# Performance work log

Hardware: AMD Instinct MI355X
Metric: run time of the kernel (lower is better)

The kernel has to match this reference:

```python
import jax, jax.numpy as jnp
import numpy as np

B, S, D = 256, 512, 128
NQ, NC, NQD, NCD = 20000, 2000, 101, 101


def setup_inputs() -> dict:
    key = jax.random.key(0)
    ks = jax.random.split(key, 32)
    s = 0.05
    inp = {
        "question_seq": jax.random.randint(ks[0], (B, S), 0, NQ),
        "concept_seq": jax.random.randint(ks[1], (B, S), 0, NC),
        "question_diff_seq": jax.random.randint(ks[2], (B, S), 0, NQD),
        "concept_diff_seq": jax.random.randint(ks[3], (B, S), 0, NCD),
        "correct_seq": jax.random.randint(ks[4], (B, S), 0, 2),
        "E_q": jax.random.normal(ks[5], (NQ, D)) * s,
        "E_c": jax.random.normal(ks[6], (NC, D)) * s,
        "E_qd": jax.random.normal(ks[7], (NQD, D)) * s,
        "E_cd": jax.random.normal(ks[8], (NCD, D)) * s,
        "E_corr": jax.random.normal(ks[9], (2, D)) * s,
        "Wx": jax.random.normal(ks[10], (4 * D, D)) * s,
        "bx": jnp.zeros((D,)),
        "W_s1": jax.random.normal(ks[11], (D, D)) * s,
        "b_s1": jnp.zeros((D,)),
        "W_s2": jax.random.normal(ks[12], (D, D)) * s,
        "b_s2": jnp.zeros((D,)),
        "W_p1": jax.random.normal(ks[13], (2 * D, D)) * s,
        "b_p1": jnp.zeros((D,)),
        "W_p2": jax.random.normal(ks[14], (2 * D, D)) * s,
        "b_p2": jnp.zeros((D,)),
        "W_ki": jax.random.normal(ks[15], (4 * D, D)) * s,
        "b_ki": jnp.zeros((D,)),
        # xavier_uniform init of h_pre: bound = sqrt(6/(fan_in+fan_out))
        "h0": jax.random.uniform(ks[16], (B, D), minval=-1.0, maxval=1.0) * np.sqrt(6.0 / (B + D)),
    }
    return inp


def reference(question_seq, concept_seq, question_diff_seq, concept_diff_seq,
              correct_seq, E_q, E_c, E_qd, E_cd, E_corr,
              Wx, bx, W_s1, b_s1, W_s2, b_s2,
              W_p1, b_p1, W_p2, b_p2, W_ki, b_ki, h0):
    # embedding lookups: [B,S,D] each
    q = E_q[question_seq]
    c = E_c[concept_seq]
    qd = E_qd[question_diff_seq]
    cd = E_cd[concept_diff_seq]
    corr = E_corr[correct_seq]
    # generate_x_MLP applied to full sequence at once (loop-invariant)
    x = jnp.concatenate([q, c, qd, cd], axis=-1) @ Wx + bx  # [B,S,D]
    # time-major inputs for the recurrence over t = 0..S-2
    xs = jnp.swapaxes(x, 0, 1)          # [S,B,D]
    corr_t = jnp.swapaxes(corr, 0, 1)   # [S,B,D]
    qd_t = jnp.swapaxes(qd, 0, 1)
    cd_t = jnp.swapaxes(cd, 0, 1)

    def step(h, inp):
        x_t, x_next, co, qdt, cdt = inp
        d = x_t - h
        sdf = jax.nn.sigmoid(d @ W_s1 + b_s1) * jnp.tanh(d @ W_s2 + b_s2)  # dropout=eval
        pk_in = jnp.concatenate([sdf, co], axis=-1)
        pka = jax.nn.sigmoid(pk_in @ W_p1 + b_p1) * jnp.tanh(pk_in @ W_p2 + b_p2)
        ki_in = jnp.concatenate([h, co, qdt, cdt], axis=-1)
        g = jax.nn.sigmoid(ki_in @ W_ki + b_ki)
        h_new = g * h + (1.0 - g) * pka
        y_t = jax.nn.sigmoid(jnp.sum(x_next * h_new, axis=-1))  # [B]
        return h_new, y_t

    scan_in = (xs[:-1], xs[1:], corr_t[:-1], qd_t[:-1], cd_t[:-1])
    _, y_body = jax.lax.scan(step, h0, scan_in)  # y_body: [S-1,B]
    y = jnp.concatenate([y_body.T, jnp.zeros((question_seq.shape[0], 1), y_body.dtype)], axis=1)
    return y  # [B,S], last column zero as in original
```

## Files before the change

### kernel.cpp

```cpp
#include <hip/hip_runtime.h>

#define BB 256
#define SS 512
#define DD 128

__device__ __forceinline__ float sigf(float v) {
    return __builtin_amdgcn_rcpf(1.0f + __expf(-v));
}
__device__ __forceinline__ float tanhf_(float v) {
    return 1.0f - 2.0f * __builtin_amdgcn_rcpf(__expf(2.0f * v) + 1.0f);
}

__device__ __forceinline__ void lds_barrier() {
    asm volatile("s_waitcnt lgkmcnt(0)" ::: "memory");
    __builtin_amdgcn_s_barrier();
}

typedef _Float16 f16x2 __attribute__((ext_vector_type(2)));
typedef _Float16 f16x8 __attribute__((ext_vector_type(8)));
typedef float    f32x4 __attribute__((ext_vector_type(4)));

#define MFMA16(A, B, C) __builtin_amdgcn_mfma_f32_16x16x32_f16((A), (B), (C), 0, 0, 0)

#define N_EQ  (20000 * 128)
#define N_EC  (2000 * 128)
#define N_EQD (101 * 128)
#define N_ECD (101 * 128)
#define N_WXT (512 * 128)
#define N_WS  (128 * 128)
#define N_CVT (N_EQ + N_EC + N_EQD + N_ECD + N_WXT + 2 * N_WS)

__global__ __launch_bounds__(256) void dimkt_cvt(
    const float* __restrict__ E_q, const float* __restrict__ E_c,
    const float* __restrict__ E_qd, const float* __restrict__ E_cd,
    const float* __restrict__ Wx,
    const float* __restrict__ W_s1, const float* __restrict__ W_s2,
    _Float16* __restrict__ E_qh, _Float16* __restrict__ E_ch,
    _Float16* __restrict__ E_qdh, _Float16* __restrict__ E_cdh,
    _Float16* __restrict__ WxTh,
    _Float16* __restrict__ Ws1T, _Float16* __restrict__ Ws2T)
{
    int o = blockIdx.x * 256 + threadIdx.x;
    if (o >= N_CVT) return;
    if (o < N_EQ) { E_qh[o] = (_Float16)E_q[o]; return; }
    o -= N_EQ;
    if (o < N_EC) { E_ch[o] = (_Float16)E_c[o]; return; }
    o -= N_EC;
    if (o < N_EQD) { E_qdh[o] = (_Float16)E_qd[o]; return; }
    o -= N_EQD;
    if (o < N_ECD) { E_cdh[o] = (_Float16)E_cd[o]; return; }
    o -= N_ECD;
    if (o < N_WXT) {
        int n = o >> 9, k = o & 511;
        WxTh[o] = (_Float16)Wx[k * 128 + n];
        return;
    }
    o -= N_WXT;
    if (o < N_WS) {
        int n = o >> 7, k = o & 127;
        Ws1T[o] = (_Float16)W_s1[k * 128 + n];
        return;
    }
    o -= N_WS;
    {
        int n = o >> 7, k = o & 127;
        Ws2T[o] = (_Float16)W_s2[k * 128 + n];
    }
}

__global__ void dimkt_tables(const float* __restrict__ E_corr,
                             const float* __restrict__ E_qd,
                             const float* __restrict__ E_cd,
                             const float* __restrict__ W_ki,
                             const float* __restrict__ W_p1,
                             const float* __restrict__ W_p2,
                             const float* __restrict__ b_ki,
                             const float* __restrict__ b_p1,
                             const float* __restrict__ b_p2,
                             float* __restrict__ Ck, float* __restrict__ Cp1,
                             float* __restrict__ Cp2, float* __restrict__ Qk,
                             float* __restrict__ Cdk)
{
    __shared__ float e[128];
    const int r = blockIdx.x;
    const int j = threadIdx.x;
    const float *emb, *W, *bias;
    float* op;
    if (r < 2)        { emb = E_corr + r * 128;        W = W_ki + 128 * 128; bias = b_ki;    op = Ck  + r * 128; }
    else if (r < 4)   { emb = E_corr + (r - 2) * 128;  W = W_p1 + 128 * 128; bias = b_p1;    op = Cp1 + (r - 2) * 128; }
    else if (r < 6)   { emb = E_corr + (r - 4) * 128;  W = W_p2 + 128 * 128; bias = b_p2;    op = Cp2 + (r - 4) * 128; }
    else if (r < 107) { emb = E_qd   + (r - 6) * 128;  W = W_ki + 256 * 128; bias = nullptr; op = Qk  + (r - 6) * 128; }
    else              { emb = E_cd   + (r - 107) * 128; W = W_ki + 384 * 128; bias = nullptr; op = Cdk + (r - 107) * 128; }
    e[j] = emb[j];
    __syncthreads();
    float acc = bias ? bias[j] : 0.0f;
#pragma unroll 8
    for (int i = 0; i < 128; ++i) acc = fmaf(e[i], W[i * 128 + j], acc);
    op[j] = acc;
}

__global__ __launch_bounds__(256, 2) void dimkt_xgemm(
    const int* __restrict__ q_seq, const int* __restrict__ c_seq,
    const int* __restrict__ qd_seq, const int* __restrict__ cd_seq,
    const _Float16* __restrict__ E_qh, const _Float16* __restrict__ E_ch,
    const _Float16* __restrict__ E_qdh, const _Float16* __restrict__ E_cdh,
    const _Float16* __restrict__ WxTh,
    const float* __restrict__ bx, _Float16* __restrict__ xh)
{
    const int tid = threadIdx.x;
    const int wv  = tid >> 6;
    const int l   = tid & 63;
    const int lm  = l & 15;
    const int kg8 = (l >> 4) * 8;
    const int m0  = blockIdx.x * 128;
    const int rbase = m0 + wv * 32;

    f32x4 acc0[8], acc1[8];
#pragma unroll
    for (int c = 0; c < 8; ++c) {
        acc0[c] = (f32x4){0.f, 0.f, 0.f, 0.f};
        acc1[c] = (f32x4){0.f, 0.f, 0.f, 0.f};
    }

#pragma unroll
    for (int s = 0; s < 4; ++s) {
        const _Float16* T  = (s == 0) ? E_qh : (s == 1) ? E_ch : (s == 2) ? E_qdh : E_cdh;
        const int*      sq = (s == 0) ? q_seq : (s == 1) ? c_seq : (s == 2) ? qd_seq : cd_seq;
        const int i0 = sq[rbase + lm];
        const int i1 = sq[rbase + 16 + lm];
        const _Float16* a0p = T + (size_t)i0 * 128 + kg8;
        const _Float16* a1p = T + (size_t)i1 * 128 + kg8;
#pragma unroll
        for (int kk = 0; kk < 4; ++kk) {
            const f16x8 a0 = *(const f16x8*)(a0p + kk * 32);
            const f16x8 a1 = *(const f16x8*)(a1p + kk * 32);
#pragma unroll
            for (int c = 0; c < 8; ++c) {
                const f16x8 bf = *(const f16x8*)&WxTh[(size_t)(c * 16 + lm) * 512
                                                      + s * 128 + kk * 32 + kg8];
                acc0[c] = MFMA16(a0, bf, acc0[c]);
                acc1[c] = MFMA16(a1, bf, acc1[c]);
            }
        }
    }

#pragma unroll
    for (int c = 0; c < 8; ++c) {
        const int col = c * 16 + lm;
        const float bxv = bx[col];
#pragma unroll
        for (int r = 0; r < 4; ++r) {
            const int row0 = rbase + (l >> 4) * 4 + r;
            xh[(size_t)row0 * 128 + col]        = (_Float16)(acc0[c][r] + bxv);
            xh[(size_t)(row0 + 16) * 128 + col] = (_Float16)(acc1[c][r] + bxv);
        }
    }
}

__global__ __launch_bounds__(256, 2) void dimkt_x12(
    const _Float16* __restrict__ xh,
    const _Float16* __restrict__ Ws1T, const _Float16* __restrict__ Ws2T,
    const float* __restrict__ b_s1, const float* __restrict__ b_s2,
    _Float16* __restrict__ X1h, _Float16* __restrict__ X2h)
{
    const int tid = threadIdx.x;
    const int wv  = tid >> 6;
    const int l   = tid & 63;
    const int lm  = l & 15;
    const int kg8 = (l >> 4) * 8;
    const int rbase = blockIdx.x * 128 + wv * 32;

    f32x4 acc0[16], acc1[16];
#pragma unroll
    for (int c = 0; c < 16; ++c) {
        acc0[c] = (f32x4){0.f, 0.f, 0.f, 0.f};
        acc1[c] = (f32x4){0.f, 0.f, 0.f, 0.f};
    }

    const _Float16* a0p = xh + (size_t)(rbase + lm) * 128 + kg8;
    const _Float16* a1p = xh + (size_t)(rbase + 16 + lm) * 128 + kg8;
#pragma unroll
    for (int kk = 0; kk < 4; ++kk) {
        const f16x8 a0 = *(const f16x8*)(a0p + kk * 32);
        const f16x8 a1 = *(const f16x8*)(a1p + kk * 32);
#pragma unroll
        for (int c = 0; c < 16; ++c) {
            const _Float16* BT = (c < 8) ? Ws1T : Ws2T;
            const f16x8 bf = *(const f16x8*)&BT[(size_t)((c & 7) * 16 + lm) * 128
                                                + kk * 32 + kg8];
            acc0[c] = MFMA16(a0, bf, acc0[c]);
            acc1[c] = MFMA16(a1, bf, acc1[c]);
        }
    }

#pragma unroll
    for (int c = 0; c < 16; ++c) {
        const int col = (c & 7) * 16 + lm;
        const float bv = (c < 8) ? b_s1[col] : b_s2[col];
        _Float16* ob = (c < 8) ? X1h : X2h;
#pragma unroll
        for (int r = 0; r < 4; ++r) {
            const int row0 = rbase + (l >> 4) * 4 + r;
            ob[(size_t)row0 * 128 + col]        = (_Float16)(acc0[c][r] + bv);
            ob[(size_t)(row0 + 16) * 128 + col] = (_Float16)(acc1[c][r] + bv);
        }
    }
}

__device__ __forceinline__ f16x8 load_wfrag(const float* __restrict__ W,
                                            int kbase, int j) {
    f16x8 r;
#pragma unroll
    for (int e = 0; e < 8; ++e) r[e] = (_Float16)W[(kbase + e) * DD + j];
    return r;
}
__device__ __forceinline__ f16x8 load_wfrag_neg(const float* __restrict__ W,
                                                int kbase, int j) {
    f16x8 r;
#pragma unroll
    for (int e = 0; e < 8; ++e) r[e] = (_Float16)(-W[(kbase + e) * DD + j]);
    return r;
}

__global__ __launch_bounds__(512, 2) void dimkt_scan(
    const _Float16* __restrict__ X1h, const _Float16* __restrict__ X2h,
    const int* __restrict__ corr_seq, const int* __restrict__ qd_seq,
    const int* __restrict__ cd_seq,
    const float* __restrict__ W_s1, const float* __restrict__ W_s2,
    const float* __restrict__ W_p1, const float* __restrict__ W_p2,
    const float* __restrict__ W_ki,
    const float* __restrict__ Ck, const float* __restrict__ Cp1,
    const float* __restrict__ Cp2, const float* __restrict__ Qk,
    const float* __restrict__ Cdk,
    const float* __restrict__ h0, _Float16* __restrict__ hb,
    float* __restrict__ out)
{
    __shared__ __align__(16) _Float16 h_h[128];
    __shared__ __align__(16) _Float16 s_h[128];

    const int tid  = threadIdx.x;
    const int b    = blockIdx.x;
    const int wv   = tid >> 6;
    const int l    = tid & 63;
    const int kgrp = l >> 4;
    const int j    = wv * 16 + (l & 15);
    const int base = b * SS;

    const int kb = kgrp * 8;
    const f16x8 w1f0 = load_wfrag_neg(W_s1,  0 + kb, j);
    const f16x8 w1f1 = load_wfrag_neg(W_s1, 32 + kb, j);
    const f16x8 w1f2 = load_wfrag_neg(W_s1, 64 + kb, j);
    const f16x8 w1f3 = load_wfrag_neg(W_s1, 96 + kb, j);
    const f16x8 w2f0 = load_wfrag_neg(W_s2,  0 + kb, j);
    const f16x8 w2f1 = load_wfrag_neg(W_s2, 32 + kb, j);
    const f16x8 w2f2 = load_wfrag_neg(W_s2, 64 + kb, j);
    const f16x8 w2f3 = load_wfrag_neg(W_s2, 96 + kb, j);
    const f16x8 wkf0 = load_wfrag(W_ki,  0 + kb, j);
    const f16x8 wkf1 = load_wfrag(W_ki, 32 + kb, j);
    const f16x8 wkf2 = load_wfrag(W_ki, 64 + kb, j);
    const f16x8 wkf3 = load_wfrag(W_ki, 96 + kb, j);
    const f16x8 p1f0 = load_wfrag(W_p1,  0 + kb, j);
    const f16x8 p1f1 = load_wfrag(W_p1, 32 + kb, j);
    const f16x8 p1f2 = load_wfrag(W_p1, 64 + kb, j);
    const f16x8 p1f3 = load_wfrag(W_p1, 96 + kb, j);
    const f16x8 p2f0 = load_wfrag(W_p2,  0 + kb, j);
    const f16x8 p2f1 = load_wfrag(W_p2, 32 + kb, j);
    const f16x8 p2f2 = load_wfrag(W_p2, 64 + kb, j);
    const f16x8 p2f3 = load_wfrag(W_p2, 96 + kb, j);

    float h = h0[b * DD + j];
    if (kgrp == 0) h_h[j] = (_Float16)h;

    int ic = __builtin_amdgcn_readfirstlane(corr_seq[base]);
    int iq = __builtin_amdgcn_readfirstlane(qd_seq[base]);
    int ie = __builtin_amdgcn_readfirstlane(cd_seq[base]);
    float tck = Ck [ic * DD + j];
    float tqk = Qk [iq * DD + j];
    float tcd = Cdk[ie * DD + j];
    float tp1 = Cp1[ic * DD + j];
    float tp2 = Cp2[ic * DD + j];
    int icN = __builtin_amdgcn_readfirstlane(corr_seq[base + 1]);
    int iqN = __builtin_amdgcn_readfirstlane(qd_seq[base + 1]);
    int ieN = __builtin_amdgcn_readfirstlane(cd_seq[base + 1]);
    float X1v = (float)X1h[(size_t)base * DD + j];
    float X2v = (float)X2h[(size_t)base * DD + j];
    lds_barrier();

    const f32x4 z = {0.f, 0.f, 0.f, 0.f};

#pragma unroll 2
    for (int t = 0; t < 511; ++t) {
        float nck = Ck [icN * DD + j];
        float nqk = Qk [iqN * DD + j];
        float ncd = Cdk[ieN * DD + j];
        float np1 = Cp1[icN * DD + j];
        float np2 = Cp2[icN * DD + j];
        const int n2 = base + ((t + 2 > 511) ? 511 : (t + 2));
        int icN2 = __builtin_amdgcn_readfirstlane(corr_seq[n2]);
        int iqN2 = __builtin_amdgcn_readfirstlane(qd_seq[n2]);
        int ieN2 = __builtin_amdgcn_readfirstlane(cd_seq[n2]);

        const f16x8 hA0 = *(const f16x8*)&h_h[ 0 + kb];
        const f16x8 hA1 = *(const f16x8*)&h_h[32 + kb];
        const f16x8 hA2 = *(const f16x8*)&h_h[64 + kb];
        const f16x8 hA3 = *(const f16x8*)&h_h[96 + kb];

        f32x4 c1a = MFMA16(hA0, w1f0, z);
        f32x4 c2a = MFMA16(hA0, w2f0, z);
        f32x4 cka = MFMA16(hA0, wkf0, z);
        f32x4 c1b = MFMA16(hA2, w1f2, z);
        f32x4 c2b = MFMA16(hA2, w2f2, z);
        f32x4 ckb = MFMA16(hA2, wkf2, z);
        c1a = MFMA16(hA1, w1f1, c1a);
        c2a = MFMA16(hA1, w2f1, c2a);
        cka = MFMA16(hA1, wkf1, cka);
        c1b = MFMA16(hA3, w1f3, c1b);
        c2b = MFMA16(hA3, w2f3, c2b);
        ckb = MFMA16(hA3, wkf3, ckb);

        float a1 = X1v + c1a[0] + c1b[0];
        float a2 = X2v + c2a[0] + c2b[0];
        float sdf = sigf(a1) * tanhf_(a2);
        if (kgrp == 0) s_h[j] = (_Float16)sdf;
        float t3 = tck + tqk + tcd;
        float kg = cka[0] + ckb[0];
        lds_barrier();

        const f16x8 sA0 = *(const f16x8*)&s_h[ 0 + kb];
        const f16x8 sA1 = *(const f16x8*)&s_h[32 + kb];
        const f16x8 sA2 = *(const f16x8*)&s_h[64 + kb];
        const f16x8 sA3 = *(const f16x8*)&s_h[96 + kb];

        f32x4 q1a = MFMA16(sA0, p1f0, z);
        f32x4 q2a = MFMA16(sA0, p2f0, z);
        f32x4 q1b = MFMA16(sA2, p1f2, z);
        f32x4 q2b = MFMA16(sA2, p2f2, z);
        q1a = MFMA16(sA1, p1f1, q1a);
        q2a = MFMA16(sA1, p2f1, q2a);
        q1b = MFMA16(sA3, p1f3, q1b);
        q2b = MFMA16(sA3, p2f3, q2b);

        float g = sigf(kg + t3);

        const size_t xoff = (size_t)(base + t + 1) * DD;
        float nX1 = (float)X1h[xoff + j];
        float nX2 = (float)X2h[xoff + j];

        float pka = sigf(q1a[0] + q1b[0] + tp1) * tanhf_(q2a[0] + q2b[0] + tp2);
        float hn  = fmaf(g, h - pka, pka);
        _Float16 hn16 = (_Float16)hn;
        if (kgrp == 0) {
            h_h[j] = hn16;
            hb[(size_t)(base + t) * DD + j] = hn16;
        }

        h = hn;
        X1v = nX1; X2v = nX2;
        tck = nck; tqk = nqk; tcd = ncd; tp1 = np1; tp2 = np2;
        icN = icN2; iqN = iqN2; ieN = ieN2;
        lds_barrier();
    }

    if (tid == 0) out[base + 511] = 0.0f;
}

__global__ __launch_bounds__(256) void dimkt_y(
    const _Float16* __restrict__ xh, const _Float16* __restrict__ hb,
    float* __restrict__ out)
{
    const int o = blockIdx.x * 4 + (threadIdx.x >> 6);
    const int l = threadIdx.x & 63;
    const int b = o >> 9;
    const int t = o & 511;
    if (t == 511) return;
    f16x2 xv = *(const f16x2*)&xh[((size_t)(b * SS + t + 1)) * DD + 2 * l];
    f16x2 hv = *(const f16x2*)&hb[((size_t)(b * SS + t)) * DD + 2 * l];
    float s = (float)xv.x * (float)hv.x + (float)xv.y * (float)hv.y;
    s += __shfl_xor(s, 1);  s += __shfl_xor(s, 2);  s += __shfl_xor(s, 4);
    s += __shfl_xor(s, 8);  s += __shfl_xor(s, 16); s += __shfl_xor(s, 32);
    if (l == 0) out[b * SS + t] = sigf(s);
}

extern "C" void kernel_launch(void* const* d_in, const int* in_sizes, int n_in,
                              void* d_out, int out_size, void* d_ws, size_t ws_size,
                              hipStream_t stream) {
    const int*   q_seq    = (const int*)d_in[0];
    const int*   c_seq    = (const int*)d_in[1];
    const int*   qd_seq   = (const int*)d_in[2];
    const int*   cd_seq   = (const int*)d_in[3];
    const int*   corr_seq = (const int*)d_in[4];
    const float* E_q    = (const float*)d_in[5];
    const float* E_c    = (const float*)d_in[6];
    const float* E_qd   = (const float*)d_in[7];
    const float* E_cd   = (const float*)d_in[8];
    const float* E_corr = (const float*)d_in[9];
    const float* Wx     = (const float*)d_in[10];
    const float* bx     = (const float*)d_in[11];
    const float* W_s1   = (const float*)d_in[12];
    const float* b_s1   = (const float*)d_in[13];
    const float* W_s2   = (const float*)d_in[14];
    const float* b_s2   = (const float*)d_in[15];
    const float* W_p1   = (const float*)d_in[16];
    const float* b_p1   = (const float*)d_in[17];
    const float* W_p2   = (const float*)d_in[18];
    const float* b_p2   = (const float*)d_in[19];
    const float* W_ki   = (const float*)d_in[20];
    const float* b_ki   = (const float*)d_in[21];
    const float* h0     = (const float*)d_in[22];
    float* out = (float*)d_out;

    float* Ck   = (float*)d_ws;
    float* Cp1  = Ck  + 256;
    float* Cp2  = Cp1 + 256;
    float* Qk   = Cp2 + 256;
    float* Cdk  = Qk  + 101 * 128;
    _Float16* pool  = (_Float16*)((char*)d_ws + (size_t)131072);
    const size_t NBT = (size_t)BB * SS * DD;
    _Float16* xh    = pool;
    _Float16* X1h   = xh  + NBT;
    _Float16* X2h   = X1h + NBT;
    _Float16* hbuf  = X2h + NBT;
    _Float16* E_qh  = hbuf + NBT;
    _Float16* E_ch  = E_qh + N_EQ;
    _Float16* E_qdh = E_ch + N_EC;
    _Float16* E_cdh = E_qdh + N_EQD;
    _Float16* WxTh  = E_cdh + N_ECD;
    _Float16* Ws1T  = WxTh + N_WXT;
    _Float16* Ws2T  = Ws1T + N_WS;

    dimkt_cvt<<<(N_CVT + 255) / 256, 256, 0, stream>>>(
        E_q, E_c, E_qd, E_cd, Wx, W_s1, W_s2,
        E_qh, E_ch, E_qdh, E_cdh, WxTh, Ws1T, Ws2T);

    dimkt_tables<<<208, 128, 0, stream>>>(E_corr, E_qd, E_cd, W_ki, W_p1, W_p2,
                                          b_ki, b_p1, b_p2, Ck, Cp1, Cp2, Qk, Cdk);

    dimkt_xgemm<<<(BB * SS) / 128, 256, 0, stream>>>(q_seq, c_seq, qd_seq, cd_seq,
                                                     E_qh, E_ch, E_qdh, E_cdh,
                                                     WxTh, bx, xh);

    dimkt_x12<<<(BB * SS) / 128, 256, 0, stream>>>(xh, Ws1T, Ws2T, b_s1, b_s2,
                                                   X1h, X2h);

    dimkt_scan<<<BB, 512, 0, stream>>>(X1h, X2h, corr_seq, qd_seq, cd_seq,
                                       W_s1, W_s2, W_p1, W_p2, W_ki,
                                       Ck, Cp1, Cp2, Qk, Cdk, h0, hbuf, out);

    dimkt_y<<<(BB * SS) / 4, 256, 0, stream>>>(xh, hbuf, out);
}
```

Baseline: 530.6 us.

## Precompute per-step gate tables and interleave X1/X2 to shorten scan loads

Adds a pre-pass kernel that sums the corr/qd/cd gate contributions into a per-timestep fp16 buffer, and packs the Cp1/Cp2 tables as fp16 pairs. It also interleaves the X1/X2 projections into one f16x2 array. The sequential scan loop then issues three loads per step instead of many dependent index-driven gathers, which shortens its per-step latency chain. The cost is an extra kernel launch, more global traffic and workspace, and fp16 rounding of the summed gate bias.

Result: no change. 521.3 us (-1.8%).

```diff
diff --git a/kernel.cpp b/kernel.cpp
--- a/kernel.cpp
+++ b/kernel.cpp
@@ -99,6 +99,30 @@
     op[j] = acc;
 }
 
+__global__ __launch_bounds__(256) void dimkt_strm(
+    const int* __restrict__ corr_seq, const int* __restrict__ qd_seq,
+    const int* __restrict__ cd_seq,
+    const float* __restrict__ Ck, const float* __restrict__ Qk,
+    const float* __restrict__ Cdk,
+    const float* __restrict__ Cp1, const float* __restrict__ Cp2,
+    _Float16* __restrict__ kgb, f16x2* __restrict__ Cp12h)
+{
+    const int row = blockIdx.x * 2 + (threadIdx.x >> 7);
+    const int j   = threadIdx.x & 127;
+    const int ic  = corr_seq[row];
+    const int iq  = qd_seq[row];
+    const int ie  = cd_seq[row];
+    float v = Ck[ic * 128 + j] + Qk[iq * 128 + j] + Cdk[ie * 128 + j];
+    kgb[(size_t)row * 128 + j] = (_Float16)v;
+    if (blockIdx.x == 0) {
+        int c = threadIdx.x >> 7, jj = threadIdx.x & 127;
+        f16x2 t;
+        t.x = (_Float16)Cp1[c * 128 + jj];
+        t.y = (_Float16)Cp2[c * 128 + jj];
+        Cp12h[c * 128 + jj] = t;
+    }
+}
+
 __global__ __launch_bounds__(256, 2) void dimkt_xgemm(
     const int* __restrict__ q_seq, const int* __restrict__ c_seq,
     const int* __restrict__ qd_seq, const int* __restrict__ cd_seq,
@@ -161,7 +185,7 @@
     const _Float16* __restrict__ xh,
     const _Float16* __restrict__ Ws1T, const _Float16* __restrict__ Ws2T,
     const float* __restrict__ b_s1, const float* __restrict__ b_s2,
-    _Float16* __restrict__ X1h, _Float16* __restrict__ X2h)
+    f16x2* __restrict__ X12)
 {
     const int tid = threadIdx.x;
     const int wv  = tid >> 6;
@@ -194,15 +218,20 @@
     }
 
 #pragma unroll
-    for (int c = 0; c < 16; ++c) {
-        const int col = (c & 7) * 16 + lm;
-        const float bv = (c < 8) ? b_s1[col] : b_s2[col];
-        _Float16* ob = (c < 8) ? X1h : X2h;
+    for (int c = 0; c < 8; ++c) {
+        const int col = c * 16 + lm;
+        const float bv1 = b_s1[col];
+        const float bv2 = b_s2[col];
 #pragma unroll
         for (int r = 0; r < 4; ++r) {
             const int row0 = rbase + (l >> 4) * 4 + r;
-            ob[(size_t)row0 * 128 + col]        = (_Float16)(acc0[c][r] + bv);
-            ob[(size_t)(row0 + 16) * 128 + col] = (_Float16)(acc1[c][r] + bv);
+            f16x2 v0, v1;
+            v0.x = (_Float16)(acc0[c][r] + bv1);
+            v0.y = (_Float16)(acc0[c + 8][r] + bv2);
+            v1.x = (_Float16)(acc1[c][r] + bv1);
+            v1.y = (_Float16)(acc1[c + 8][r] + bv2);
+            X12[(size_t)row0 * 128 + col]        = v0;
+            X12[(size_t)(row0 + 16) * 128 + col] = v1;
         }
     }
 }
@@ -223,15 +252,11 @@
 }
 
 __global__ __launch_bounds__(512, 2) void dimkt_scan(
-    const _Float16* __restrict__ X1h, const _Float16* __restrict__ X2h,
-    const int* __restrict__ corr_seq, const int* __restrict__ qd_seq,
-    const int* __restrict__ cd_seq,
+    const f16x2* __restrict__ X12, const _Float16* __restrict__ kgb,
+    const int* __restrict__ corr_seq, const f16x2* __restrict__ Cp12h,
     const float* __restrict__ W_s1, const float* __restrict__ W_s2,
     const float* __restrict__ W_p1, const float* __restrict__ W_p2,
     const float* __restrict__ W_ki,
-    const float* __restrict__ Ck, const float* __restrict__ Cp1,
-    const float* __restrict__ Cp2, const float* __restrict__ Qk,
-    const float* __restrict__ Cdk,
     const float* __restrict__ h0, _Float16* __restrict__ hb,
     float* __restrict__ out)
 {
@@ -271,35 +296,16 @@
     float h = h0[b * DD + j];
     if (kgrp == 0) h_h[j] = (_Float16)h;
 
-    int ic = __builtin_amdgcn_readfirstlane(corr_seq[base]);
-    int iq = __builtin_amdgcn_readfirstlane(qd_seq[base]);
-    int ie = __builtin_amdgcn_readfirstlane(cd_seq[base]);
-    float tck = Ck [ic * DD + j];
-    float tqk = Qk [iq * DD + j];
-    float tcd = Cdk[ie * DD + j];
-    float tp1 = Cp1[ic * DD + j];
-    float tp2 = Cp2[ic * DD + j];
+    f16x2    X12v = X12[(size_t)base * DD + j];
+    _Float16 kgt  = kgb[(size_t)base * DD + j];
+    f16x2    cpv  = Cp12h[corr_seq[base] * DD + j];
     int icN = __builtin_amdgcn_readfirstlane(corr_seq[base + 1]);
-    int iqN = __builtin_amdgcn_readfirstlane(qd_seq[base + 1]);
-    int ieN = __builtin_amdgcn_readfirstlane(cd_seq[base + 1]);
-    float X1v = (float)X1h[(size_t)base * DD + j];
-    float X2v = (float)X2h[(size_t)base * DD + j];
     lds_barrier();
 
     const f32x4 z = {0.f, 0.f, 0.f, 0.f};
 
 #pragma unroll 2
     for (int t = 0; t < 511; ++t) {
-        float nck = Ck [icN * DD + j];
-        float nqk = Qk [iqN * DD + j];
-        float ncd = Cdk[ieN * DD + j];
-        float np1 = Cp1[icN * DD + j];
-        float np2 = Cp2[icN * DD + j];
-        const int n2 = base + ((t + 2 > 511) ? 511 : (t + 2));
-        int icN2 = __builtin_amdgcn_readfirstlane(corr_seq[n2]);
-        int iqN2 = __builtin_amdgcn_readfirstlane(qd_seq[n2]);
-        int ieN2 = __builtin_amdgcn_readfirstlane(cd_seq[n2]);
-
         const f16x8 hA0 = *(const f16x8*)&h_h[ 0 + kb];
         const f16x8 hA1 = *(const f16x8*)&h_h[32 + kb];
         const f16x8 hA2 = *(const f16x8*)&h_h[64 + kb];
@@ -318,12 +324,11 @@
         c2b = MFMA16(hA3, w2f3, c2b);
         ckb = MFMA16(hA3, wkf3, ckb);
 
-        float a1 = X1v + c1a[0] + c1b[0];
-        float a2 = X2v + c2a[0] + c2b[0];
+        float a1 = (float)X12v.x + c1a[0] + c1b[0];
+        float a2 = (float)X12v.y + c2a[0] + c2b[0];
         float sdf = sigf(a1) * tanhf_(a2);
         if (kgrp == 0) s_h[j] = (_Float16)sdf;
-        float t3 = tck + tqk + tcd;
-        float kg = cka[0] + ckb[0];
+        float kg = cka[0] + ckb[0] + (float)kgt;
         lds_barrier();
 
         const f16x8 sA0 = *(const f16x8*)&s_h[ 0 + kb];
@@ -340,13 +345,17 @@
         q1b = MFMA16(sA3, p1f3, q1b);
         q2b = MFMA16(sA3, p2f3, q2b);
 
-        float g = sigf(kg + t3);
-
-        const size_t xoff = (size_t)(base + t + 1) * DD;
-        float nX1 = (float)X1h[xoff + j];
-        float nX2 = (float)X2h[xoff + j];
-
-        float pka = sigf(q1a[0] + q1b[0] + tp1) * tanhf_(q2a[0] + q2b[0] + tp2);
+        float g = sigf(kg);
+
+        const size_t noff = (size_t)(base + t + 1) * DD + j;
+        f16x2    nX12 = X12[noff];
+        _Float16 nkgt = kgb[noff];
+        f16x2    ncp  = Cp12h[icN * DD + j];
+        const int n2 = base + ((t + 2 > 511) ? 511 : (t + 2));
+        int icN2 = __builtin_amdgcn_readfirstlane(corr_seq[n2]);
+
+        float pka = sigf(q1a[0] + q1b[0] + (float)cpv.x)
+                  * tanhf_(q2a[0] + q2b[0] + (float)cpv.y);
         float hn  = fmaf(g, h - pka, pka);
         _Float16 hn16 = (_Float16)hn;
         if (kgrp == 0) {
@@ -355,9 +364,7 @@
         }
 
         h = hn;
-        X1v = nX1; X2v = nX2;
-        tck = nck; tqk = nqk; tcd = ncd; tp1 = np1; tp2 = np2;
-        icN = icN2; iqN = iqN2; ieN = ieN2;
+        X12v = nX12; kgt = nkgt; cpv = ncp; icN = icN2;
         lds_barrier();
     }
 
@@ -417,10 +424,11 @@
     _Float16* pool  = (_Float16*)((char*)d_ws + (size_t)131072);
     const size_t NBT = (size_t)BB * SS * DD;
     _Float16* xh    = pool;
-    _Float16* X1h   = xh  + NBT;
-    _Float16* X2h   = X1h + NBT;
-    _Float16* hbuf  = X2h + NBT;
-    _Float16* E_qh  = hbuf + NBT;
+    f16x2*    X12   = (f16x2*)(xh + NBT);
+    _Float16* hbuf  = (_Float16*)(X12 + NBT);
+    _Float16* kgb   = hbuf + NBT;
+    f16x2*    Cp12h = (f16x2*)(kgb + NBT);
+    _Float16* E_qh  = (_Float16*)(Cp12h + 256);
     _Float16* E_ch  = E_qh + N_EQ;
     _Float16* E_qdh = E_ch + N_EC;
     _Float16* E_cdh = E_qdh + N_EQD;
@@ -435,16 +443,20 @@
     dimkt_tables<<<208, 128, 0, stream>>>(E_corr, E_qd, E_cd, W_ki, W_p1, W_p2,
                                           b_ki, b_p1, b_p2, Ck, Cp1, Cp2, Qk, Cdk);
 
+    dimkt_strm<<<(BB * SS) / 2, 256, 0, stream>>>(corr_seq, qd_seq, cd_seq,
+                                                  Ck, Qk, Cdk, Cp1, Cp2,
+                                                  kgb, Cp12h);
+
     dimkt_xgemm<<<(BB * SS) / 128, 256, 0, stream>>>(q_seq, c_seq, qd_seq, cd_seq,
                                                      E_qh, E_ch, E_qdh, E_cdh,
                                                      WxTh, bx, xh);
 
     dimkt_x12<<<(BB * SS) / 128, 256, 0, stream>>>(xh, Ws1T, Ws2T, b_s1, b_s2,
-                                                   X1h, X2h);
-
-    dimkt_scan<<<BB, 512, 0, stream>>>(X1h, X2h, corr_seq, qd_seq, cd_seq,
+                                                   X12);
+
+    dimkt_scan<<<BB, 512, 0, stream>>>(X12, kgb, corr_seq, Cp12h,
                                        W_s1, W_s2, W_p1, W_p2, W_ki,
-                                       Ck, Cp1, Cp2, Qk, Cdk, h0, hbuf, out);
+                                       h0, hbuf, out);
 
     dimkt_y<<<(BB * SS) / 4, 256, 0, stream>>>(xh, hbuf, out);
 }
```
